# Kernel optimization log

Hardware: AMD Instinct MI355X
Metric: run time of the kernel (lower is better)

Reference implementation:

```python
import jax, jax.numpy as jnp
import numpy as np
import math

B, N, M, O = 64, 2048, 64, 128  # batch, neurons, in_dims, out_dims


def setup_inputs() -> dict:
    key = jax.random.key(0)
    kx, kw, kb = jax.random.split(key, 3)
    s = 1.0 / math.sqrt(M + O)
    x = jax.random.normal(kx, (B, N, M), dtype=jnp.float32)
    # master weights fp32, init U(-s, s) as in the torch module
    w1 = jax.random.uniform(kw, (M, O, N), dtype=jnp.float32, minval=-s, maxval=s)
    b1 = jnp.zeros((1, N, O), dtype=jnp.float32)
    return {"x": x, "w1": w1, "b1": b1}


def reference(x, w1, b1):
    # N independent per-neuron linears: [B,N,M] x [M,O,N] -> [B,N,O]
    # cast master weights/bias to compute dtype (matches .to(x.dtype))
    w = w1.astype(x.dtype)
    b = b1.astype(x.dtype)
    return jnp.einsum('bnm,mon->bno', x, w) + b
```

## Files before the change

kernel.cpp:

```cpp
#include <hip/hip_runtime.h>
#include <hip/hip_bf16.h>

#define N_TOT 2048
#define M_DIM 64
#define O_DIM 128
#define NT 8
#define OC 32

typedef __bf16 bf16x8 __attribute__((ext_vector_type(8)));
typedef float f32x4 __attribute__((ext_vector_type(4)));

__global__ __launch_bounds__(256, 4) void superlinear_mfma(
    const float* __restrict__ x, const float* __restrict__ w1,
    const float* __restrict__ b1, float* __restrict__ out)
{
    __shared__ unsigned char wlds[NT * OC * M_DIM * 2];

    const int tid  = threadIdx.x;
    const int lane = tid & 63;
    const int wave = tid >> 6;

    const int bid = blockIdx.x;
    const int swz = (bid & 7) * 128 + (bid >> 3);
    const int nq  = swz >> 2;
    const int oq  = swz & 3;
    const int n0  = nq * NT;
    const int o0  = oq * OC;

    const int col = lane & 15;
    const int kg  = lane >> 4;

    const int half = tid & 1;
    const int ol   = (tid >> 1) & 31;
    const int mseg = tid >> 6;

    const size_t MSTR = (size_t)O_DIM * N_TOT;

    float4 sr[16];
    {
        const float* gp = w1 + ((size_t)(mseg * 16) * O_DIM + (o0 + ol)) * N_TOT
                             + n0 + half * 4;
        #pragma unroll
        for (int mm = 0; mm < 16; ++mm)
            sr[mm] = *(const float4*)(gp + (size_t)mm * MSTR);
    }

    float bv[2][2];
    #pragma unroll
    for (int n2 = 0; n2 < 2; ++n2)
        #pragma unroll
        for (int ot = 0; ot < 2; ++ot)
            bv[n2][ot] = b1[(size_t)(n0 + wave * 2 + n2) * O_DIM + o0 + ot * 16 + col];

    float4 xr[8];
    auto load_x = [&](int bt, float4* r) {
        #pragma unroll
        for (int n2 = 0; n2 < 2; ++n2)
            #pragma unroll
            for (int kc = 0; kc < 2; ++kc) {
                const float* xp = x
                    + ((size_t)(bt * 16 + col) * N_TOT + (n0 + wave * 2 + n2)) * M_DIM
                    + kc * 32 + kg * 8;
                r[n2 * 4 + kc * 2 + 0] = *(const float4*)xp;
                r[n2 * 4 + kc * 2 + 1] = *(const float4*)(xp + 4);
            }
    };
    load_x(0, xr);

    #pragma unroll
    for (int j = 0; j < 4; ++j) {
        int nn = half * 4 + j;
        #pragma unroll
        for (int q = 0; q < 2; ++q) {
            bf16x8 v;
            #pragma unroll
            for (int t = 0; t < 8; ++t)
                v[t] = (__bf16)(((const float*)&sr[q * 8 + t])[j]);
            unsigned addr = (unsigned)(nn * 4096 + ol * 128 + mseg * 32 + q * 16);
            addr ^= (unsigned)((ol & 7) << 4);
            *(bf16x8*)(wlds + addr) = v;
        }
    }

    __syncthreads();

    const unsigned sw = (unsigned)(col & 7) << 4;
    #pragma unroll
    for (int bt = 0; bt < 4; ++bt) {
        bf16x8 af[2][2];
        #pragma unroll
        for (int n2 = 0; n2 < 2; ++n2)
            #pragma unroll
            for (int kc = 0; kc < 2; ++kc) {
                const float* lp = (const float*)&xr[n2 * 4 + kc * 2 + 0];
                const float* hp = (const float*)&xr[n2 * 4 + kc * 2 + 1];
                bf16x8 v;
                #pragma unroll
                for (int t = 0; t < 4; ++t) {
                    v[t]     = (__bf16)lp[t];
                    v[4 + t] = (__bf16)hp[t];
                }
                af[n2][kc] = v;
            }
        if (bt < 3) load_x(bt + 1, xr);

        #pragma unroll
        for (int n2 = 0; n2 < 2; ++n2) {
            int nn = wave * 2 + n2;
            int n  = n0 + nn;
            f32x4 aa[2];
            #pragma unroll
            for (int ot = 0; ot < 2; ++ot) {
                unsigned la = (unsigned)(nn * 4096 + (ot * 16 + col) * 128 + kg * 16);
                bf16x8 bf0 = *(const bf16x8*)(wlds + (la ^ sw));
                bf16x8 bf1 = *(const bf16x8*)(wlds + ((la + 64) ^ sw));
                f32x4 ci;
                float b0 = bv[n2][ot];
                ci[0] = b0; ci[1] = b0; ci[2] = b0; ci[3] = b0;
                aa[ot] = __builtin_amdgcn_mfma_f32_16x16x32_bf16(af[n2][0], bf0, ci,     0, 0, 0);
                aa[ot] = __builtin_amdgcn_mfma_f32_16x16x32_bf16(af[n2][1], bf1, aa[ot], 0, 0, 0);
            }
            #pragma unroll
            for (int r = 0; r < 4; ++r) {
                int b = bt * 16 + kg * 4 + r;
                float* op = out + ((size_t)b * N_TOT + n) * O_DIM + o0 + col;
                op[0]  = aa[0][r];
                op[16] = aa[1][r];
            }
        }
    }
}

extern "C" void kernel_launch(void* const* d_in, const int* in_sizes, int n_in,
                              void* d_out, int out_size, void* d_ws, size_t ws_size,
                              hipStream_t stream) {
    const float* x  = (const float*)d_in[0];
    const float* w1 = (const float*)d_in[1];
    const float* b1 = (const float*)d_in[2];
    float* out = (float*)d_out;
    superlinear_mfma<<<dim3(1024), dim3(256), 0, stream>>>(x, w1, b1, out);
}
```

Measured before the change: 36.28 us.

## Enlarge block tile to 32 neurons by 64 outputs with K split in two phases

Reorganizes the kernel so each 512-thread block handles 32 neurons, 64 output columns and half the batch. The weight tile is staged through LDS in two K-halves with fully coalesced 32-byte segments along N, and accumulators live in registers across both phases. The grid shrinks from 1024 to 256 blocks. The intent is wider global weight reads per row and fewer blocks, at the cost of weights now being loaded twice (once per batch half), an extra barrier, higher register pressure, and dropping the LDS XOR swizzle, which may cause bank conflicts.

```diff
diff --git a/kernel.cpp b/kernel.cpp
--- a/kernel.cpp
+++ b/kernel.cpp
@@ -4,130 +4,136 @@
 #define N_TOT 2048
 #define M_DIM 64
 #define O_DIM 128
-#define NT 8
-#define OC 32
+#define NT 32
+#define OC 64
 
 typedef __bf16 bf16x8 __attribute__((ext_vector_type(8)));
 typedef float f32x4 __attribute__((ext_vector_type(4)));
 
-__global__ __launch_bounds__(256, 4) void superlinear_mfma(
+__global__ __launch_bounds__(512, 2) void superlinear_mfma(
     const float* __restrict__ x, const float* __restrict__ w1,
     const float* __restrict__ b1, float* __restrict__ out)
 {
-    __shared__ unsigned char wlds[NT * OC * M_DIM * 2];
+    __shared__ unsigned char wlds[NT * OC * 32 * 2];
 
     const int tid  = threadIdx.x;
     const int lane = tid & 63;
     const int wave = tid >> 6;
 
     const int bid = blockIdx.x;
-    const int swz = (bid & 7) * 128 + (bid >> 3);
-    const int nq  = swz >> 2;
-    const int oq  = swz & 3;
-    const int n0  = nq * NT;
-    const int o0  = oq * OC;
+    const int swz = (bid & 7) * 32 + (bid >> 3);
+    const int ng  = swz >> 2;
+    const int oh  = (swz >> 1) & 1;
+    const int bh  = swz & 1;
+    const int n0  = ng * NT;
+    const int o0  = oh * OC;
+    const int b0  = bh * 32;
 
     const int col = lane & 15;
     const int kg  = lane >> 4;
 
-    const int half = tid & 1;
-    const int ol   = (tid >> 1) & 31;
-    const int mseg = tid >> 6;
+    const int n8 = tid & 7;
+    const int ol = (tid >> 3) & 63;
 
     const size_t MSTR = (size_t)O_DIM * N_TOT;
 
-    float4 sr[16];
-    {
-        const float* gp = w1 + ((size_t)(mseg * 16) * O_DIM + (o0 + ol)) * N_TOT
-                             + n0 + half * 4;
+    f32x4 acc[4][2][4];
+    #pragma unroll
+    for (int n2 = 0; n2 < 4; ++n2) {
+        int n = n0 + wave * 4 + n2;
         #pragma unroll
-        for (int mm = 0; mm < 16; ++mm)
-            sr[mm] = *(const float4*)(gp + (size_t)mm * MSTR);
-    }
-
-    float bv[2][2];
-    #pragma unroll
-    for (int n2 = 0; n2 < 2; ++n2)
-        #pragma unroll
-        for (int ot = 0; ot < 2; ++ot)
-            bv[n2][ot] = b1[(size_t)(n0 + wave * 2 + n2) * O_DIM + o0 + ot * 16 + col];
-
-    float4 xr[8];
-    auto load_x = [&](int bt, float4* r) {
-        #pragma unroll
-        for (int n2 = 0; n2 < 2; ++n2)
+        for (int ot = 0; ot < 4; ++ot) {
+            float bvv = b1[(size_t)n * O_DIM + o0 + ot * 16 + col];
             #pragma unroll
-            for (int kc = 0; kc < 2; ++kc) {
-                const float* xp = x
-                    + ((size_t)(bt * 16 + col) * N_TOT + (n0 + wave * 2 + n2)) * M_DIM
-                    + kc * 32 + kg * 8;
-                r[n2 * 4 + kc * 2 + 0] = *(const float4*)xp;
-                r[n2 * 4 + kc * 2 + 1] = *(const float4*)(xp + 4);
+            for (int bt = 0; bt < 2; ++bt) {
+                acc[n2][bt][ot][0] = bvv; acc[n2][bt][ot][1] = bvv;
+                acc[n2][bt][ot][2] = bvv; acc[n2][bt][ot][3] = bvv;
             }
-    };
-    load_x(0, xr);
-
-    #pragma unroll
-    for (int j = 0; j < 4; ++j) {
-        int nn = half * 4 + j;
-        #pragma unroll
-        for (int q = 0; q < 2; ++q) {
-            bf16x8 v;
-            #pragma unroll
-            for (int t = 0; t < 8; ++t)
-                v[t] = (__bf16)(((const float*)&sr[q * 8 + t])[j]);
-            unsigned addr = (unsigned)(nn * 4096 + ol * 128 + mseg * 32 + q * 16);
-            addr ^= (unsigned)((ol & 7) << 4);
-            *(bf16x8*)(wlds + addr) = v;
         }
     }
 
-    __syncthreads();
+    #pragma unroll
+    for (int p = 0; p < 2; ++p) {
+        float4 xr[4][2][2];
+        #pragma unroll
+        for (int n2 = 0; n2 < 4; ++n2)
+            #pragma unroll
+            for (int bt = 0; bt < 2; ++bt) {
+                const float* xp = x
+                    + ((size_t)(b0 + bt * 16 + col) * N_TOT + (n0 + wave * 4 + n2)) * M_DIM
+                    + p * 32 + kg * 8;
+                xr[n2][bt][0] = *(const float4*)xp;
+                xr[n2][bt][1] = *(const float4*)(xp + 4);
+            }
 
-    const unsigned sw = (unsigned)(col & 7) << 4;
-    #pragma unroll
-    for (int bt = 0; bt < 4; ++bt) {
-        bf16x8 af[2][2];
         #pragma unroll
-        for (int n2 = 0; n2 < 2; ++n2)
+        for (int sb = 0; sb < 4; ++sb) {
+            float4 r[8];
+            const float* gp = w1 + ((size_t)(p * 32 + sb * 8) * O_DIM + (o0 + ol)) * N_TOT
+                                 + n0 + n8 * 4;
             #pragma unroll
-            for (int kc = 0; kc < 2; ++kc) {
-                const float* lp = (const float*)&xr[n2 * 4 + kc * 2 + 0];
-                const float* hp = (const float*)&xr[n2 * 4 + kc * 2 + 1];
+            for (int mm = 0; mm < 8; ++mm)
+                r[mm] = *(const float4*)(gp + (size_t)mm * MSTR);
+            #pragma unroll
+            for (int j = 0; j < 4; ++j) {
+                int nn = n8 * 4 + j;
+                bf16x8 v;
+                #pragma unroll
+                for (int mm = 0; mm < 8; ++mm)
+                    v[mm] = (__bf16)(((const float*)&r[mm])[j]);
+                *(bf16x8*)(wlds + (unsigned)(nn * 4096 + ol * 64 + sb * 16)) = v;
+            }
+        }
+
+        bf16x8 af[4][2];
+        #pragma unroll
+        for (int n2 = 0; n2 < 4; ++n2)
+            #pragma unroll
+            for (int bt = 0; bt < 2; ++bt) {
+                const float* lp = (const float*)&xr[n2][bt][0];
+                const float* hp = (const float*)&xr[n2][bt][1];
                 bf16x8 v;
                 #pragma unroll
                 for (int t = 0; t < 4; ++t) {
                     v[t]     = (__bf16)lp[t];
                     v[4 + t] = (__bf16)hp[t];
                 }
-                af[n2][kc] = v;
+                af[n2][bt] = v;
             }
-        if (bt < 3) load_x(bt + 1, xr);
+
+        __syncthreads();
 
         #pragma unroll
-        for (int n2 = 0; n2 < 2; ++n2) {
-            int nn = wave * 2 + n2;
-            int n  = n0 + nn;
-            f32x4 aa[2];
+        for (int n2 = 0; n2 < 4; ++n2) {
+            int nn = wave * 4 + n2;
             #pragma unroll
-            for (int ot = 0; ot < 2; ++ot) {
-                unsigned la = (unsigned)(nn * 4096 + (ot * 16 + col) * 128 + kg * 16);
-                bf16x8 bf0 = *(const bf16x8*)(wlds + (la ^ sw));
-                bf16x8 bf1 = *(const bf16x8*)(wlds + ((la + 64) ^ sw));
-                f32x4 ci;
-                float b0 = bv[n2][ot];
-                ci[0] = b0; ci[1] = b0; ci[2] = b0; ci[3] = b0;
-                aa[ot] = __builtin_amdgcn_mfma_f32_16x16x32_bf16(af[n2][0], bf0, ci,     0, 0, 0);
-                aa[ot] = __builtin_amdgcn_mfma_f32_16x16x32_bf16(af[n2][1], bf1, aa[ot], 0, 0, 0);
-            }
-            #pragma unroll
-            for (int r = 0; r < 4; ++r) {
-                int b = bt * 16 + kg * 4 + r;
-                float* op = out + ((size_t)b * N_TOT + n) * O_DIM + o0 + col;
-                op[0]  = aa[0][r];
-                op[16] = aa[1][r];
+            for (int ot = 0; ot < 4; ++ot) {
+                bf16x8 bfrag = *(const bf16x8*)(wlds
+                    + (unsigned)(nn * 4096 + (ot * 16 + col) * 64 + kg * 16));
+                #pragma unroll
+                for (int bt = 0; bt < 2; ++bt)
+                    acc[n2][bt][ot] = __builtin_amdgcn_mfma_f32_16x16x32_bf16(
+                        af[n2][bt], bfrag, acc[n2][bt][ot], 0, 0, 0);
             }
         }
+
+        if (p == 0) __syncthreads();
+    }
+
+    #pragma unroll
+    for (int n2 = 0; n2 < 4; ++n2) {
+        int n = n0 + wave * 4 + n2;
+        #pragma unroll
+        for (int bt = 0; bt < 2; ++bt)
+            #pragma unroll
+            for (int j = 0; j < 4; ++j) {
+                int b = b0 + bt * 16 + kg * 4 + j;
+                float* op = out + ((size_t)b * N_TOT + n) * O_DIM + o0 + col;
+                op[0]  = acc[n2][bt][0][j];
+                op[16] = acc[n2][bt][1][j];
+                op[32] = acc[n2][bt][2][j];
+                op[48] = acc[n2][bt][3][j];
+            }
     }
 }
 
@@ -138,5 +144,5 @@
     const float* w1 = (const float*)d_in[1];
     const float* b1 = (const float*)d_in[2];
     float* out = (float*)d_out;
-    superlinear_mfma<<<dim3(1024), dim3(256), 0, stream>>>(x, w1, b1, out);
+    superlinear_mfma<<<dim3(256), dim3(512), 0, stream>>>(x, w1, b1, out);
 }
```

Result: slower. 39.23 us (+8.1%).
